# Optimization experiments

Hardware: AMD Instinct MI355X
Metric: run time of the kernel (lower is better)

Reference implementation:

```python
import jax, jax.numpy as jnp
import numpy as np

COMMITMENT_COST = 0.25


def setup_inputs() -> dict:
    key = jax.random.key(0)
    k1, k2 = jax.random.split(key)
    B, S, D, K = 8, 4096, 256, 1024
    inputs = jax.random.normal(k1, (B, S, D), dtype=jnp.float32)
    attention_mask = jnp.ones((B, S), dtype=jnp.float32)
    codebook = jax.random.normal(k2, (K, D), dtype=jnp.float32)
    return {"inputs": inputs, "attention_mask": attention_mask, "codebook": codebook}


def reference(inputs, attention_mask, codebook):
    # Inference-mode forward of VectorQuantizer (no EMA update / init / revival).
    B, S, D = inputs.shape
    z = inputs.astype(jnp.float32).reshape(-1, D)          # (N, D)
    m = attention_mask.reshape(-1).astype(jnp.float32)     # (N,)

    cb = codebook.astype(jnp.float32)                      # (K, D)
    # squared L2 distances: ||z||^2 - 2 z e^T + ||e||^2
    dist = (jnp.sum(z * z, axis=-1, keepdims=True)
            - 2.0 * jnp.matmul(z, cb.T)
            + jnp.sum(cb * cb, axis=-1)[None, :])          # (N, K)
    idx = jnp.argmin(dist, axis=-1)                        # (N,)
    q = cb[idx]                                            # (N, D) codebook lookup

    n_valid = jnp.sum(m)
    # mse over valid tokens (elementwise mean, matching F.mse_loss on flat_valid)
    diff = z - jax.lax.stop_gradient(q)
    commitment = jnp.sum(m[:, None] * diff * diff) / (n_valid * D)
    vq_loss = COMMITMENT_COST * commitment

    # straight-through estimator; invalid positions zeroed (as in torch scatter)
    q_ste = z + jax.lax.stop_gradient(q - z)
    quantized = (q_ste * m[:, None]).reshape(B, S, D)
    indices = jnp.where(m > 0, idx, 0).reshape(B, S)
    return quantized, vq_loss, indices
```

## Files before the change

kernel.cpp:

```cpp
#include <hip/hip_runtime.h>
#include <cstdint>

typedef short bf16x8 __attribute__((ext_vector_type(8)));
typedef float f32x4  __attribute__((ext_vector_type(4)));

#define TOK    64
#define PITCH  264
#define HROWS  (64 * PITCH)
#define MAXC   32

__device__ __forceinline__ unsigned short f2bf(float f) {
  unsigned u = __float_as_uint(f);
  return (unsigned short)((u + 0x7FFFu + ((u >> 16) & 1u)) >> 16);
}
__device__ __forceinline__ uint4 pack8(float4 a, float4 b) {
  uint4 u;
  u.x = (unsigned)f2bf(a.x) | ((unsigned)f2bf(a.y) << 16);
  u.y = (unsigned)f2bf(a.z) | ((unsigned)f2bf(a.w) << 16);
  u.z = (unsigned)f2bf(b.x) | ((unsigned)f2bf(b.y) << 16);
  u.w = (unsigned)f2bf(b.z) | ((unsigned)f2bf(b.w) << 16);
  return u;
}

__global__ __launch_bounds__(256) void vq_prep(const float* __restrict__ cb,
                                               unsigned short* __restrict__ cb_bf,
                                               float* __restrict__ ee,
                                               float* __restrict__ acc2,
                                               int* __restrict__ done_ctr, int K) {
  if (blockIdx.x == 0 && threadIdx.x == 0) {
    acc2[0] = 0.f; acc2[1] = 0.f; *done_ctr = 0;
  }
  int wave = threadIdx.x >> 6, lane = threadIdx.x & 63;
  int k = blockIdx.x * 4 + wave;
  if (k >= K) return;
  float4 v = *reinterpret_cast<const float4*>(cb + (size_t)k * 256 + lane * 4);
  float s = v.x * v.x + v.y * v.y + v.z * v.z + v.w * v.w;
  #pragma unroll
  for (int off = 32; off; off >>= 1) s += __shfl_down(s, off, 64);
  ushort4 b;
  b.x = f2bf(v.x); b.y = f2bf(v.y); b.z = f2bf(v.z); b.w = f2bf(v.w);
  *reinterpret_cast<ushort4*>(cb_bf + (size_t)k * 256 + lane * 4) = b;
  if (lane == 0) ee[k] = s;
}

__global__ __launch_bounds__(256, 2) void vq_main(
    const float* __restrict__ z, const float* __restrict__ cb,
    const unsigned short* __restrict__ cb_bf, const float* __restrict__ ee,
    const float* __restrict__ mask,
    float* __restrict__ out_q, float* __restrict__ out_idx_f,
    float* __restrict__ out_loss, float* __restrict__ acc2,
    int* __restrict__ done_ctr, int nblocks, int K) {
  __shared__ __align__(16) unsigned short buf[128 * PITCH];
  __shared__ float ee_lds[1024];
  __shared__ float znorm[TOK];
  __shared__ int   ccnt[TOK];
  __shared__ unsigned short cand[TOK * MAXC];
  __shared__ float red[8];
  __shared__ bool  last;

  const int t = threadIdx.x;
  const int n0 = blockIdx.x * TOK;
  const int q16 = t & 15;

  ee_lds[t]       = ee[t];
  ee_lds[t + 256] = ee[t + 256];
  ee_lds[t + 512] = ee[t + 512];
  ee_lds[t + 768] = ee[t + 768];
  if (t < TOK) ccnt[t] = 0;

  #pragma unroll
  for (int pass = 0; pass < 4; ++pass) {
    int row = pass * 16 + (t >> 4);
    const float* zr = z + (size_t)(n0 + row) * 256;
    float ssq = 0.f;
    #pragma unroll
    for (int j = 0; j < 2; ++j) {
      float4 a = *reinterpret_cast<const float4*>(zr + q16 * 8 + j * 128);
      float4 b = *reinterpret_cast<const float4*>(zr + q16 * 8 + j * 128 + 4);
      ssq += a.x*a.x + a.y*a.y + a.z*a.z + a.w*a.w
           + b.x*b.x + b.y*b.y + b.z*b.z + b.w*b.w;
      *reinterpret_cast<uint4*>(&buf[row * PITCH + q16 * 8 + j * 128]) = pack8(a, b);
    }
    #pragma unroll
    for (int off = 1; off < 16; off <<= 1) ssq += __shfl_xor(ssq, off, 64);
    if (q16 == 0) znorm[row] = sqrtf(ssq);
  }
  __syncthreads();

  const int wv = t >> 6, lane = t & 63;
  const int p = wv & 1, kh = wv >> 1;
  const int quad = lane >> 4, l15 = lane & 15;
  bf16x8 afrag[2][8];
  float  znreg[2][4];
  #pragma unroll
  for (int s = 0; s < 2; ++s) {
    const unsigned short* za = &buf[(p * 32 + s * 16 + l15) * PITCH + quad * 8];
    #pragma unroll
    for (int kk = 0; kk < 8; ++kk)
      afrag[s][kk] = *reinterpret_cast<const bf16x8*>(za + kk * 32);
    #pragma unroll
    for (int r = 0; r < 4; ++r)
      znreg[s][r] = znorm[p * 32 + s * 16 + quad * 4 + r];
  }
  __syncthreads();

  float amin[2][4];
  #pragma unroll
  for (int s = 0; s < 2; ++s)
    #pragma unroll
    for (int r = 0; r < 4; ++r) amin[s][r] = 3.4e38f;

  const int tq = (p << 6) | lane;
  const int sq16 = tq & 15, srow = tq >> 4;
  unsigned short* qbuf = &buf[kh * HROWS];

  for (int lc = 0; lc < 8; ++lc) {
    const int kbase = kh * 512 + lc * 64;
    #pragma unroll
    for (int pass = 0; pass < 8; ++pass) {
      int row = pass * 8 + srow;
      const unsigned short* src = cb_bf + (size_t)(kbase + row) * 256;
      #pragma unroll
      for (int j = 0; j < 2; ++j) {
        uint4 v = *reinterpret_cast<const uint4*>(src + sq16 * 8 + j * 128);
        *reinterpret_cast<uint4*>(&qbuf[row * PITCH + sq16 * 8 + j * 128]) = v;
      }
    }
    __syncthreads();

    f32x4 acc[2][4];
    #pragma unroll
    for (int s = 0; s < 2; ++s)
      #pragma unroll
      for (int ct = 0; ct < 4; ++ct) acc[s][ct] = (f32x4){0.f, 0.f, 0.f, 0.f};
    #pragma unroll
    for (int kk = 0; kk < 8; ++kk) {
      bf16x8 b0 = *reinterpret_cast<const bf16x8*>(&qbuf[(l15)      * PITCH + quad * 8 + kk * 32]);
      bf16x8 b1 = *reinterpret_cast<const bf16x8*>(&qbuf[(16 + l15) * PITCH + quad * 8 + kk * 32]);
      bf16x8 b2 = *reinterpret_cast<const bf16x8*>(&qbuf[(32 + l15) * PITCH + quad * 8 + kk * 32]);
      bf16x8 b3 = *reinterpret_cast<const bf16x8*>(&qbuf[(48 + l15) * PITCH + quad * 8 + kk * 32]);
      acc[0][0] = __builtin_amdgcn_mfma_f32_16x16x32_bf16(afrag[0][kk], b0, acc[0][0], 0, 0, 0);
      acc[1][0] = __builtin_amdgcn_mfma_f32_16x16x32_bf16(afrag[1][kk], b0, acc[1][0], 0, 0, 0);
      acc[0][1] = __builtin_amdgcn_mfma_f32_16x16x32_bf16(afrag[0][kk], b1, acc[0][1], 0, 0, 0);
      acc[1][1] = __builtin_amdgcn_mfma_f32_16x16x32_bf16(afrag[1][kk], b1, acc[1][1], 0, 0, 0);
      acc[0][2] = __builtin_amdgcn_mfma_f32_16x16x32_bf16(afrag[0][kk], b2, acc[0][2], 0, 0, 0);
      acc[1][2] = __builtin_amdgcn_mfma_f32_16x16x32_bf16(afrag[1][kk], b2, acc[1][2], 0, 0, 0);
      acc[0][3] = __builtin_amdgcn_mfma_f32_16x16x32_bf16(afrag[0][kk], b3, acc[0][3], 0, 0, 0);
      acc[1][3] = __builtin_amdgcn_mfma_f32_16x16x32_bf16(afrag[1][kk], b3, acc[1][3], 0, 0, 0);
    }

    float e0 = ee_lds[kbase + l15],      e1 = ee_lds[kbase + 16 + l15];
    float e2 = ee_lds[kbase + 32 + l15], e3 = ee_lds[kbase + 48 + l15];
    float en0 = sqrtf(e0), en1 = sqrtf(e1), en2 = sqrtf(e2), en3 = sqrtf(e3);
    #pragma unroll
    for (int s = 0; s < 2; ++s) {
      #pragma unroll
      for (int r = 0; r < 4; ++r) {
        float d0 = e0 - 2.f * acc[s][0][r];
        float d1 = e1 - 2.f * acc[s][1][r];
        float d2 = e2 - 2.f * acc[s][2][r];
        float d3 = e3 - 2.f * acc[s][3][r];
        float w = fminf(fminf(d0, d1), fminf(d2, d3));
        #pragma unroll
        for (int off = 1; off < 16; off <<= 1) w = fminf(w, __shfl_xor(w, off, 64));
        float am = fminf(amin[s][r], w);
        amin[s][r] = am;
        int tok = p * 32 + s * 16 + quad * 4 + r;
        float zn = znreg[s][r];
        if (d0 <= am + 1.5f + 0.002f * zn * en0) {
          int sl = atomicAdd(&ccnt[tok], 1);
          if (sl < MAXC) cand[tok * MAXC + sl] = (unsigned short)(kbase + l15);
        }
        if (d1 <= am + 1.5f + 0.002f * zn * en1) {
          int sl = atomicAdd(&ccnt[tok], 1);
          if (sl < MAXC) cand[tok * MAXC + sl] = (unsigned short)(kbase + 16 + l15);
        }
        if (d2 <= am + 1.5f + 0.002f * zn * en2) {
          int sl = atomicAdd(&ccnt[tok], 1);
          if (sl < MAXC) cand[tok * MAXC + sl] = (unsigned short)(kbase + 32 + l15);
        }
        if (d3 <= am + 1.5f + 0.002f * zn * en3) {
          int sl = atomicAdd(&ccnt[tok], 1);
          if (sl < MAXC) cand[tok * MAXC + sl] = (unsigned short)(kbase + 48 + l15);
        }
      }
    }
    __syncthreads();
  }

  float lsum = 0.f, msum = 0.f;
  for (int it = 0; it < 16; ++it) {
    int tok = wv * 16 + it;
    int n = n0 + tok;
    float4 zv = *reinterpret_cast<const float4*>(z + (size_t)n * 256 + lane * 4);
    int cnt = ccnt[tok];
    float bs = 3.4e38f; int bk = 0;
    if (cnt > MAXC) {
      for (int k = 0; k < K; ++k) {
        float4 ev = *reinterpret_cast<const float4*>(cb + (size_t)k * 256 + lane * 4);
        float dp = zv.x * ev.x + zv.y * ev.y + zv.z * ev.z + zv.w * ev.w;
        #pragma unroll
        for (int off = 32; off; off >>= 1) dp += __shfl_xor(dp, off, 64);
        float s = ee_lds[k] - 2.f * dp;
        if (s < bs) { bs = s; bk = k; }
      }
    } else {
      for (int c = 0; c < cnt; ++c) {
        int k = cand[tok * MAXC + c];
        float4 ev = *reinterpret_cast<const float4*>(cb + (size_t)k * 256 + lane * 4);
        float dp = zv.x * ev.x + zv.y * ev.y + zv.z * ev.z + zv.w * ev.w;
        #pragma unroll
        for (int off = 32; off; off >>= 1) dp += __shfl_xor(dp, off, 64);
        float s = ee_lds[k] - 2.f * dp;
        if (s < bs || (s == bs && k < bk)) { bs = s; bk = k; }
      }
    }
    float m = mask[n];
    float4 qv = *reinterpret_cast<const float4*>(cb + (size_t)bk * 256 + lane * 4);
    float4 o; o.x = qv.x * m; o.y = qv.y * m; o.z = qv.z * m; o.w = qv.w * m;
    *reinterpret_cast<float4*>(out_q + (size_t)n * 256 + lane * 4) = o;
    float dx = zv.x - qv.x, dy = zv.y - qv.y, dz = zv.z - qv.z, dw = zv.w - qv.w;
    lsum = fmaf(m, dx * dx + dy * dy + dz * dz + dw * dw, lsum);
    if (lane == 0) {
      msum += m;
      out_idx_f[n] = (m > 0.f) ? (float)bk : 0.f;
    }
  }
  #pragma unroll
  for (int off = 32; off; off >>= 1) lsum += __shfl_down(lsum, off, 64);
  if (lane == 0) { red[wv] = lsum; red[4 + wv] = msum; }
  __syncthreads();
  if (t == 0) {
    atomicAdd(&acc2[0], red[0] + red[1] + red[2] + red[3]);
    atomicAdd(&acc2[1], red[4] + red[5] + red[6] + red[7]);
    __threadfence();
    int prev = atomicAdd(done_ctr, 1);
    last = (prev == nblocks - 1);
  }
  __syncthreads();
  if (last && t == 0) {
    float s  = atomicAdd(&acc2[0], 0.0f);
    float nv = atomicAdd(&acc2[1], 0.0f);
    out_loss[0] = (nv > 0.f) ? (0.25f * s / (nv * 256.0f)) : 0.0f;
  }
}

extern "C" void kernel_launch(void* const* d_in, const int* in_sizes, int n_in,
                              void* d_out, int out_size, void* d_ws, size_t ws_size,
                              hipStream_t stream) {
  const float* z    = (const float*)d_in[0];
  const float* mask = (const float*)d_in[1];
  const float* cb   = (const float*)d_in[2];
  const int N = in_sizes[1];
  const int D = 256;
  const int K = in_sizes[2] / D;

  float* wsf  = (float*)d_ws;
  float* acc2 = wsf;
  int*   dctr = (int*)(wsf + 2);
  float* ee   = wsf + 8;
  unsigned short* cb_bf = (unsigned short*)(ee + K);

  float* out_q     = (float*)d_out;
  float* out_loss  = out_q + (size_t)N * D;
  float* out_idx_f = out_loss + 1;

  vq_prep<<<(K + 3) / 4, 256, 0, stream>>>(cb, cb_bf, ee, acc2, dctr, K);
  vq_main<<<N / TOK, 256, 0, stream>>>(z, cb, cb_bf, ee, mask, out_q,
                                       out_idx_f, out_loss, acc2, dctr, N / TOK, K);
}
```

Before: 194.0 us.

## Double block to 512 threads, prefetch codebook tiles, and prune refine candidates

Blocks grow to 512 threads (8 waves), and each wave now owns 16 tokens with one fragment set instead of 32. Codebook tiles are prefetched into registers one chunk ahead so global loads overlap the MFMA work, and MFMA sections run at raised wave priority. Candidate entries now pack a truncated distance with the index, and a shared atomicMin tracks each token's running best. The refine pass drops candidates beyond a threshold and skips exact recomputation when only one survives. This cuts the exact fp32 refine work, but adds LDS atomics and a heuristic threshold that could affect argmin correctness on close ties.

```diff
diff --git a/kernel.cpp b/kernel.cpp
--- a/kernel.cpp
+++ b/kernel.cpp
@@ -7,7 +7,7 @@
 #define TOK    64
 #define PITCH  264
 #define HROWS  (64 * PITCH)
-#define MAXC   32
+#define MAXC   24
 
 __device__ __forceinline__ unsigned short f2bf(float f) {
   unsigned u = __float_as_uint(f);
@@ -43,7 +43,7 @@
   if (lane == 0) ee[k] = s;
 }
 
-__global__ __launch_bounds__(256, 2) void vq_main(
+__global__ __launch_bounds__(512, 2) void vq_main(
     const float* __restrict__ z, const float* __restrict__ cb,
     const unsigned short* __restrict__ cb_bf, const float* __restrict__ ee,
     const float* __restrict__ mask,
@@ -54,32 +54,38 @@
   __shared__ float ee_lds[1024];
   __shared__ float znorm[TOK];
   __shared__ int   ccnt[TOK];
-  __shared__ unsigned short cand[TOK * MAXC];
-  __shared__ float red[8];
+  __shared__ unsigned umin[TOK];
+  __shared__ unsigned cand[TOK * MAXC];
+  __shared__ float red[16];
   __shared__ bool  last;
 
   const int t = threadIdx.x;
   const int n0 = blockIdx.x * TOK;
+  const int wv = t >> 6, lane = t & 63;
+  const int kh = wv >> 2, ts = wv & 3;
+  const int quad = lane >> 4, l15 = lane & 15;
   const int q16 = t & 15;
 
-  ee_lds[t]       = ee[t];
-  ee_lds[t + 256] = ee[t + 256];
-  ee_lds[t + 512] = ee[t + 512];
-  ee_lds[t + 768] = ee[t + 768];
-  if (t < TOK) ccnt[t] = 0;
-
-  #pragma unroll
-  for (int pass = 0; pass < 4; ++pass) {
-    int row = pass * 16 + (t >> 4);
+  float ea = ee[t], eb = ee[t + 512];
+  ee_lds[t] = ea; ee_lds[t + 512] = eb;
+  if (t < TOK) { ccnt[t] = 0; umin[t] = 0x7F7FFC00u; }
+  float em = fmaxf(ea, eb);
+  #pragma unroll
+  for (int off = 32; off; off >>= 1) em = fmaxf(em, __shfl_xor(em, off, 64));
+  if (lane == 0) red[wv] = em;
+
+  #pragma unroll
+  for (int pass = 0; pass < 2; ++pass) {
+    int row = pass * 32 + (t >> 4);
     const float* zr = z + (size_t)(n0 + row) * 256;
     float ssq = 0.f;
     #pragma unroll
     for (int j = 0; j < 2; ++j) {
-      float4 a = *reinterpret_cast<const float4*>(zr + q16 * 8 + j * 128);
-      float4 b = *reinterpret_cast<const float4*>(zr + q16 * 8 + j * 128 + 4);
+      float4 a = *reinterpret_cast<const float4*>(zr + q16 * 16 + j * 8);
+      float4 b = *reinterpret_cast<const float4*>(zr + q16 * 16 + j * 8 + 4);
       ssq += a.x*a.x + a.y*a.y + a.z*a.z + a.w*a.w
            + b.x*b.x + b.y*b.y + b.z*b.z + b.w*b.w;
-      *reinterpret_cast<uint4*>(&buf[row * PITCH + q16 * 8 + j * 128]) = pack8(a, b);
+      *reinterpret_cast<uint4*>(&buf[row * PITCH + q16 * 16 + j * 8]) = pack8(a, b);
     }
     #pragma unroll
     for (int off = 1; off < 16; off <<= 1) ssq += __shfl_xor(ssq, off, 64);
@@ -87,115 +93,132 @@
   }
   __syncthreads();
 
-  const int wv = t >> 6, lane = t & 63;
-  const int p = wv & 1, kh = wv >> 1;
-  const int quad = lane >> 4, l15 = lane & 15;
-  bf16x8 afrag[2][8];
-  float  znreg[2][4];
-  #pragma unroll
-  for (int s = 0; s < 2; ++s) {
-    const unsigned short* za = &buf[(p * 32 + s * 16 + l15) * PITCH + quad * 8];
+  float enmax;
+  {
+    float m8 = red[0];
+    #pragma unroll
+    for (int i = 1; i < 8; ++i) m8 = fmaxf(m8, red[i]);
+    enmax = sqrtf(m8);
+  }
+
+  const int tt = t & 255;
+  const unsigned short* cbh = cb_bf + (size_t)kh * 512 * 256;
+  uint4 st[8];
+  #pragma unroll
+  for (int u = 0; u < 8; ++u)
+    st[u] = *reinterpret_cast<const uint4*>(cbh + (size_t)(u * 256 + tt) * 8);
+
+  bf16x8 afrag[8];
+  float  znreg[4];
+  {
+    const unsigned short* za = &buf[(ts * 16 + l15) * PITCH + quad * 8];
     #pragma unroll
     for (int kk = 0; kk < 8; ++kk)
-      afrag[s][kk] = *reinterpret_cast<const bf16x8*>(za + kk * 32);
+      afrag[kk] = *reinterpret_cast<const bf16x8*>(za + kk * 32);
     #pragma unroll
     for (int r = 0; r < 4; ++r)
-      znreg[s][r] = znorm[p * 32 + s * 16 + quad * 4 + r];
-  }
-  __syncthreads();
-
-  float amin[2][4];
-  #pragma unroll
-  for (int s = 0; s < 2; ++s)
-    #pragma unroll
-    for (int r = 0; r < 4; ++r) amin[s][r] = 3.4e38f;
-
-  const int tq = (p << 6) | lane;
-  const int sq16 = tq & 15, srow = tq >> 4;
+      znreg[r] = znorm[ts * 16 + quad * 4 + r];
+  }
+  __syncthreads();
+
   unsigned short* qbuf = &buf[kh * HROWS];
+  #pragma unroll
+  for (int u = 0; u < 8; ++u) {
+    int f = u * 256 + tt;
+    *reinterpret_cast<uint4*>(&qbuf[(f >> 5) * PITCH + (f & 31) * 8]) = st[u];
+  }
+  __syncthreads();
+
+  float amin[4] = {3.4e38f, 3.4e38f, 3.4e38f, 3.4e38f};
 
   for (int lc = 0; lc < 8; ++lc) {
     const int kbase = kh * 512 + lc * 64;
-    #pragma unroll
-    for (int pass = 0; pass < 8; ++pass) {
-      int row = pass * 8 + srow;
-      const unsigned short* src = cb_bf + (size_t)(kbase + row) * 256;
+    if (lc < 7) {
+      const unsigned short* src = cbh + (size_t)(lc + 1) * 64 * 256;
       #pragma unroll
-      for (int j = 0; j < 2; ++j) {
-        uint4 v = *reinterpret_cast<const uint4*>(src + sq16 * 8 + j * 128);
-        *reinterpret_cast<uint4*>(&qbuf[row * PITCH + sq16 * 8 + j * 128]) = v;
-      }
-    }
-    __syncthreads();
-
-    f32x4 acc[2][4];
-    #pragma unroll
-    for (int s = 0; s < 2; ++s)
-      #pragma unroll
-      for (int ct = 0; ct < 4; ++ct) acc[s][ct] = (f32x4){0.f, 0.f, 0.f, 0.f};
+      for (int u = 0; u < 8; ++u)
+        st[u] = *reinterpret_cast<const uint4*>(src + (size_t)(u * 256 + tt) * 8);
+    }
+
+    f32x4 acc[4];
+    #pragma unroll
+    for (int ct = 0; ct < 4; ++ct) acc[ct] = (f32x4){0.f, 0.f, 0.f, 0.f};
+    __builtin_amdgcn_s_setprio(1);
     #pragma unroll
     for (int kk = 0; kk < 8; ++kk) {
       bf16x8 b0 = *reinterpret_cast<const bf16x8*>(&qbuf[(l15)      * PITCH + quad * 8 + kk * 32]);
       bf16x8 b1 = *reinterpret_cast<const bf16x8*>(&qbuf[(16 + l15) * PITCH + quad * 8 + kk * 32]);
       bf16x8 b2 = *reinterpret_cast<const bf16x8*>(&qbuf[(32 + l15) * PITCH + quad * 8 + kk * 32]);
       bf16x8 b3 = *reinterpret_cast<const bf16x8*>(&qbuf[(48 + l15) * PITCH + quad * 8 + kk * 32]);
-      acc[0][0] = __builtin_amdgcn_mfma_f32_16x16x32_bf16(afrag[0][kk], b0, acc[0][0], 0, 0, 0);
-      acc[1][0] = __builtin_amdgcn_mfma_f32_16x16x32_bf16(afrag[1][kk], b0, acc[1][0], 0, 0, 0);
-      acc[0][1] = __builtin_amdgcn_mfma_f32_16x16x32_bf16(afrag[0][kk], b1, acc[0][1], 0, 0, 0);
-      acc[1][1] = __builtin_amdgcn_mfma_f32_16x16x32_bf16(afrag[1][kk], b1, acc[1][1], 0, 0, 0);
-      acc[0][2] = __builtin_amdgcn_mfma_f32_16x16x32_bf16(afrag[0][kk], b2, acc[0][2], 0, 0, 0);
-      acc[1][2] = __builtin_amdgcn_mfma_f32_16x16x32_bf16(afrag[1][kk], b2, acc[1][2], 0, 0, 0);
-      acc[0][3] = __builtin_amdgcn_mfma_f32_16x16x32_bf16(afrag[0][kk], b3, acc[0][3], 0, 0, 0);
-      acc[1][3] = __builtin_amdgcn_mfma_f32_16x16x32_bf16(afrag[1][kk], b3, acc[1][3], 0, 0, 0);
-    }
+      acc[0] = __builtin_amdgcn_mfma_f32_16x16x32_bf16(afrag[kk], b0, acc[0], 0, 0, 0);
+      acc[1] = __builtin_amdgcn_mfma_f32_16x16x32_bf16(afrag[kk], b1, acc[1], 0, 0, 0);
+      acc[2] = __builtin_amdgcn_mfma_f32_16x16x32_bf16(afrag[kk], b2, acc[2], 0, 0, 0);
+      acc[3] = __builtin_amdgcn_mfma_f32_16x16x32_bf16(afrag[kk], b3, acc[3], 0, 0, 0);
+    }
+    __builtin_amdgcn_s_setprio(0);
 
     float e0 = ee_lds[kbase + l15],      e1 = ee_lds[kbase + 16 + l15];
     float e2 = ee_lds[kbase + 32 + l15], e3 = ee_lds[kbase + 48 + l15];
     float en0 = sqrtf(e0), en1 = sqrtf(e1), en2 = sqrtf(e2), en3 = sqrtf(e3);
     #pragma unroll
-    for (int s = 0; s < 2; ++s) {
+    for (int r = 0; r < 4; ++r) {
+      float d0 = e0 - 2.f * acc[0][r];
+      float d1 = e1 - 2.f * acc[1][r];
+      float d2 = e2 - 2.f * acc[2][r];
+      float d3 = e3 - 2.f * acc[3][r];
+      float w = fminf(fminf(d0, d1), fminf(d2, d3));
       #pragma unroll
-      for (int r = 0; r < 4; ++r) {
-        float d0 = e0 - 2.f * acc[s][0][r];
-        float d1 = e1 - 2.f * acc[s][1][r];
-        float d2 = e2 - 2.f * acc[s][2][r];
-        float d3 = e3 - 2.f * acc[s][3][r];
-        float w = fminf(fminf(d0, d1), fminf(d2, d3));
-        #pragma unroll
-        for (int off = 1; off < 16; off <<= 1) w = fminf(w, __shfl_xor(w, off, 64));
-        float am = fminf(amin[s][r], w);
-        amin[s][r] = am;
-        int tok = p * 32 + s * 16 + quad * 4 + r;
-        float zn = znreg[s][r];
-        if (d0 <= am + 1.5f + 0.002f * zn * en0) {
-          int sl = atomicAdd(&ccnt[tok], 1);
-          if (sl < MAXC) cand[tok * MAXC + sl] = (unsigned short)(kbase + l15);
-        }
-        if (d1 <= am + 1.5f + 0.002f * zn * en1) {
-          int sl = atomicAdd(&ccnt[tok], 1);
-          if (sl < MAXC) cand[tok * MAXC + sl] = (unsigned short)(kbase + 16 + l15);
-        }
-        if (d2 <= am + 1.5f + 0.002f * zn * en2) {
-          int sl = atomicAdd(&ccnt[tok], 1);
-          if (sl < MAXC) cand[tok * MAXC + sl] = (unsigned short)(kbase + 32 + l15);
-        }
-        if (d3 <= am + 1.5f + 0.002f * zn * en3) {
-          int sl = atomicAdd(&ccnt[tok], 1);
-          if (sl < MAXC) cand[tok * MAXC + sl] = (unsigned short)(kbase + 48 + l15);
-        }
+      for (int off = 1; off < 16; off <<= 1) w = fminf(w, __shfl_xor(w, off, 64));
+      int tok = ts * 16 + quad * 4 + r;
+      float gq = __uint_as_float(umin[tok] & 0xFFFFFC00u);
+      float am = fminf(fminf(amin[r], w), gq);
+      amin[r] = am;
+      float zn = znreg[r];
+      if (d0 <= am + 1.63f + 0.002f * zn * en0) {
+        unsigned pu = (__float_as_uint(fmaxf(d0, 0.f)) & 0xFFFFFC00u) | (unsigned)(kbase + l15);
+        atomicMin(&umin[tok], pu);
+        int sl = atomicAdd(&ccnt[tok], 1);
+        if (sl < MAXC) cand[tok * MAXC + sl] = pu;
+      }
+      if (d1 <= am + 1.63f + 0.002f * zn * en1) {
+        unsigned pu = (__float_as_uint(fmaxf(d1, 0.f)) & 0xFFFFFC00u) | (unsigned)(kbase + 16 + l15);
+        atomicMin(&umin[tok], pu);
+        int sl = atomicAdd(&ccnt[tok], 1);
+        if (sl < MAXC) cand[tok * MAXC + sl] = pu;
+      }
+      if (d2 <= am + 1.63f + 0.002f * zn * en2) {
+        unsigned pu = (__float_as_uint(fmaxf(d2, 0.f)) & 0xFFFFFC00u) | (unsigned)(kbase + 32 + l15);
+        atomicMin(&umin[tok], pu);
+        int sl = atomicAdd(&ccnt[tok], 1);
+        if (sl < MAXC) cand[tok * MAXC + sl] = pu;
+      }
+      if (d3 <= am + 1.63f + 0.002f * zn * en3) {
+        unsigned pu = (__float_as_uint(fmaxf(d3, 0.f)) & 0xFFFFFC00u) | (unsigned)(kbase + 48 + l15);
+        atomicMin(&umin[tok], pu);
+        int sl = atomicAdd(&ccnt[tok], 1);
+        if (sl < MAXC) cand[tok * MAXC + sl] = pu;
       }
     }
     __syncthreads();
+    if (lc < 7) {
+      #pragma unroll
+      for (int u = 0; u < 8; ++u) {
+        int f = u * 256 + tt;
+        *reinterpret_cast<uint4*>(&qbuf[(f >> 5) * PITCH + (f & 31) * 8]) = st[u];
+      }
+      __syncthreads();
+    }
   }
 
   float lsum = 0.f, msum = 0.f;
-  for (int it = 0; it < 16; ++it) {
-    int tok = wv * 16 + it;
+  for (int it = 0; it < 8; ++it) {
+    int tok = wv * 8 + it;
     int n = n0 + tok;
     float4 zv = *reinterpret_cast<const float4*>(z + (size_t)n * 256 + lane * 4);
     int cnt = ccnt[tok];
-    float bs = 3.4e38f; int bk = 0;
+    int bk = 0;
     if (cnt > MAXC) {
+      float bs = 3.4e38f;
       for (int k = 0; k < K; ++k) {
         float4 ev = *reinterpret_cast<const float4*>(cb + (size_t)k * 256 + lane * 4);
         float dp = zv.x * ev.x + zv.y * ev.y + zv.z * ev.z + zv.w * ev.w;
@@ -205,14 +228,29 @@
         if (s < bs) { bs = s; bk = k; }
       }
     } else {
-      for (int c = 0; c < cnt; ++c) {
-        int k = cand[tok * MAXC + c];
-        float4 ev = *reinterpret_cast<const float4*>(cb + (size_t)k * 256 + lane * 4);
-        float dp = zv.x * ev.x + zv.y * ev.y + zv.z * ev.z + zv.w * ev.w;
-        #pragma unroll
-        for (int off = 32; off; off >>= 1) dp += __shfl_xor(dp, off, 64);
-        float s = ee_lds[k] - 2.f * dp;
-        if (s < bs || (s == bs && k < bk)) { bs = s; bk = k; }
+      unsigned pm = umin[tok];
+      float thr = __uint_as_float(pm & 0xFFFFFC00u)
+                + 1.63f + 0.002f * znorm[tok] * enmax;
+      int c = (lane < cnt) ? lane : 0;
+      unsigned pe = cand[tok * MAXC + c];
+      bool flag = (lane < cnt) && (__uint_as_float(pe & 0xFFFFFC00u) <= thr);
+      unsigned long long msk = __ballot(flag);
+      if (__popcll(msk) == 1) {
+        bk = (int)(pm & 1023u);
+      } else {
+        float bs = 3.4e38f; bk = 1 << 29;
+        while (msk) {
+          int cc = __ffsll(msk) - 1;
+          msk &= msk - 1;
+          unsigned pc = cand[tok * MAXC + cc];
+          int k = (int)(pc & 1023u);
+          float4 ev = *reinterpret_cast<const float4*>(cb + (size_t)k * 256 + lane * 4);
+          float dp = zv.x * ev.x + zv.y * ev.y + zv.z * ev.z + zv.w * ev.w;
+          #pragma unroll
+          for (int off = 32; off; off >>= 1) dp += __shfl_xor(dp, off, 64);
+          float s = ee_lds[k] - 2.f * dp;
+          if (s < bs || (s == bs && k < bk)) { bs = s; bk = k; }
+        }
       }
     }
     float m = mask[n];
@@ -228,11 +266,14 @@
   }
   #pragma unroll
   for (int off = 32; off; off >>= 1) lsum += __shfl_down(lsum, off, 64);
-  if (lane == 0) { red[wv] = lsum; red[4 + wv] = msum; }
+  if (lane == 0) { red[wv] = lsum; red[8 + wv] = msum; }
   __syncthreads();
   if (t == 0) {
-    atomicAdd(&acc2[0], red[0] + red[1] + red[2] + red[3]);
-    atomicAdd(&acc2[1], red[4] + red[5] + red[6] + red[7]);
+    float a = 0.f, b = 0.f;
+    #pragma unroll
+    for (int i = 0; i < 8; ++i) { a += red[i]; b += red[8 + i]; }
+    atomicAdd(&acc2[0], a);
+    atomicAdd(&acc2[1], b);
     __threadfence();
     int prev = atomicAdd(done_ctr, 1);
     last = (prev == nblocks - 1);
@@ -266,6 +307,6 @@
   float* out_idx_f = out_loss + 1;
 
   vq_prep<<<(K + 3) / 4, 256, 0, stream>>>(cb, cb_bf, ee, acc2, dctr, K);
-  vq_main<<<N / TOK, 256, 0, stream>>>(z, cb, cb_bf, ee, mask, out_q,
+  vq_main<<<N / TOK, 512, 0, stream>>>(z, cb, cb_bf, ee, mask, out_q,
                                        out_idx_f, out_loss, acc2, dctr, N / TOK, K);
 }
```

Result: slower. 201.7 us (+4.0%).

## Shrink LDS tile, share packed running minimum, and prune fp32 refinement candidates

Applied to the files above, without the earlier changes.

Halves the codebook staging tile to 32 rows per chunk and drops the LDS copy of codebook norms, cutting shared memory so more blocks can reside per CU. A packed distance-plus-index value in LDS, updated with atomicMin, shares the running minimum between the two waves covering each token. In the epilogue, candidates are filtered against a global threshold, and when only one survives its index is taken directly without an fp32 recheck. This trades more loop iterations and LDS atomics, plus a slightly wider tolerance margin, for less exact fp32 refinement work.

```diff
diff --git a/kernel.cpp b/kernel.cpp
--- a/kernel.cpp
+++ b/kernel.cpp
@@ -6,8 +6,8 @@
 
 #define TOK    64
 #define PITCH  264
-#define HROWS  (64 * PITCH)
-#define MAXC   32
+#define CROWS  32
+#define MAXC   16
 
 __device__ __forceinline__ unsigned short f2bf(float f) {
   unsigned u = __float_as_uint(f);
@@ -50,23 +50,27 @@
     float* __restrict__ out_q, float* __restrict__ out_idx_f,
     float* __restrict__ out_loss, float* __restrict__ acc2,
     int* __restrict__ done_ctr, int nblocks, int K) {
-  __shared__ __align__(16) unsigned short buf[128 * PITCH];
-  __shared__ float ee_lds[1024];
+  __shared__ __align__(16) unsigned short buf[64 * PITCH];
   __shared__ float znorm[TOK];
   __shared__ int   ccnt[TOK];
-  __shared__ unsigned short cand[TOK * MAXC];
+  __shared__ unsigned umin[TOK];
+  __shared__ unsigned cand[TOK * MAXC];
   __shared__ float red[8];
   __shared__ bool  last;
 
   const int t = threadIdx.x;
   const int n0 = blockIdx.x * TOK;
+  const int wv = t >> 6, lane = t & 63;
+  const int p = wv & 1, kh = wv >> 1;
+  const int quad = lane >> 4, l15 = lane & 15;
   const int q16 = t & 15;
 
-  ee_lds[t]       = ee[t];
-  ee_lds[t + 256] = ee[t + 256];
-  ee_lds[t + 512] = ee[t + 512];
-  ee_lds[t + 768] = ee[t + 768];
-  if (t < TOK) ccnt[t] = 0;
+  if (t < TOK) { ccnt[t] = 0; umin[t] = 0x7F7FFC00u; }
+
+  float em = fmaxf(fmaxf(ee[t], ee[t + 256]), fmaxf(ee[t + 512], ee[t + 768]));
+  #pragma unroll
+  for (int off = 32; off; off >>= 1) em = fmaxf(em, __shfl_xor(em, off, 64));
+  if (lane == 0) red[wv] = em;
 
   #pragma unroll
   for (int pass = 0; pass < 4; ++pass) {
@@ -87,9 +91,8 @@
   }
   __syncthreads();
 
-  const int wv = t >> 6, lane = t & 63;
-  const int p = wv & 1, kh = wv >> 1;
-  const int quad = lane >> 4, l15 = lane & 15;
+  const float enmax = sqrtf(fmaxf(fmaxf(red[0], red[1]), fmaxf(red[2], red[3])));
+
   bf16x8 afrag[2][8];
   float  znreg[2][4];
   #pragma unroll
@@ -104,84 +107,79 @@
   }
   __syncthreads();
 
+  unsigned short* qbuf = &buf[kh * CROWS * PITCH];
+  const unsigned short* cbh = cb_bf + (size_t)kh * 512 * 256;
+  const int tq = t & 127;
+
   float amin[2][4];
   #pragma unroll
   for (int s = 0; s < 2; ++s)
     #pragma unroll
     for (int r = 0; r < 4; ++r) amin[s][r] = 3.4e38f;
 
-  const int tq = (p << 6) | lane;
-  const int sq16 = tq & 15, srow = tq >> 4;
-  unsigned short* qbuf = &buf[kh * HROWS];
-
-  for (int lc = 0; lc < 8; ++lc) {
-    const int kbase = kh * 512 + lc * 64;
-    #pragma unroll
-    for (int pass = 0; pass < 8; ++pass) {
-      int row = pass * 8 + srow;
-      const unsigned short* src = cb_bf + (size_t)(kbase + row) * 256;
-      #pragma unroll
-      for (int j = 0; j < 2; ++j) {
-        uint4 v = *reinterpret_cast<const uint4*>(src + sq16 * 8 + j * 128);
-        *reinterpret_cast<uint4*>(&qbuf[row * PITCH + sq16 * 8 + j * 128]) = v;
+  for (int lc = 0; lc < 16; ++lc) {
+    const int kbase = kh * 512 + lc * CROWS;
+    #pragma unroll
+    for (int g = 0; g < 2; ++g) {
+      uint4 v[4];
+      #pragma unroll
+      for (int u = 0; u < 4; ++u) {
+        int flat = (g * 4 + u) * 128 + tq;
+        v[u] = *reinterpret_cast<const uint4*>(
+            cbh + (size_t)(lc * CROWS + (flat >> 5)) * 256 + (flat & 31) * 8);
+      }
+      #pragma unroll
+      for (int u = 0; u < 4; ++u) {
+        int flat = (g * 4 + u) * 128 + tq;
+        *reinterpret_cast<uint4*>(&qbuf[(flat >> 5) * PITCH + (flat & 31) * 8]) = v[u];
       }
     }
     __syncthreads();
 
-    f32x4 acc[2][4];
+    f32x4 acc[2][2];
     #pragma unroll
     for (int s = 0; s < 2; ++s)
       #pragma unroll
-      for (int ct = 0; ct < 4; ++ct) acc[s][ct] = (f32x4){0.f, 0.f, 0.f, 0.f};
+      for (int ct = 0; ct < 2; ++ct) acc[s][ct] = (f32x4){0.f, 0.f, 0.f, 0.f};
+    __builtin_amdgcn_s_setprio(1);
     #pragma unroll
     for (int kk = 0; kk < 8; ++kk) {
       bf16x8 b0 = *reinterpret_cast<const bf16x8*>(&qbuf[(l15)      * PITCH + quad * 8 + kk * 32]);
       bf16x8 b1 = *reinterpret_cast<const bf16x8*>(&qbuf[(16 + l15) * PITCH + quad * 8 + kk * 32]);
-      bf16x8 b2 = *reinterpret_cast<const bf16x8*>(&qbuf[(32 + l15) * PITCH + quad * 8 + kk * 32]);
-      bf16x8 b3 = *reinterpret_cast<const bf16x8*>(&qbuf[(48 + l15) * PITCH + quad * 8 + kk * 32]);
       acc[0][0] = __builtin_amdgcn_mfma_f32_16x16x32_bf16(afrag[0][kk], b0, acc[0][0], 0, 0, 0);
       acc[1][0] = __builtin_amdgcn_mfma_f32_16x16x32_bf16(afrag[1][kk], b0, acc[1][0], 0, 0, 0);
       acc[0][1] = __builtin_amdgcn_mfma_f32_16x16x32_bf16(afrag[0][kk], b1, acc[0][1], 0, 0, 0);
       acc[1][1] = __builtin_amdgcn_mfma_f32_16x16x32_bf16(afrag[1][kk], b1, acc[1][1], 0, 0, 0);
-      acc[0][2] = __builtin_amdgcn_mfma_f32_16x16x32_bf16(afrag[0][kk], b2, acc[0][2], 0, 0, 0);
-      acc[1][2] = __builtin_amdgcn_mfma_f32_16x16x32_bf16(afrag[1][kk], b2, acc[1][2], 0, 0, 0);
-      acc[0][3] = __builtin_amdgcn_mfma_f32_16x16x32_bf16(afrag[0][kk], b3, acc[0][3], 0, 0, 0);
-      acc[1][3] = __builtin_amdgcn_mfma_f32_16x16x32_bf16(afrag[1][kk], b3, acc[1][3], 0, 0, 0);
-    }
-
-    float e0 = ee_lds[kbase + l15],      e1 = ee_lds[kbase + 16 + l15];
-    float e2 = ee_lds[kbase + 32 + l15], e3 = ee_lds[kbase + 48 + l15];
-    float en0 = sqrtf(e0), en1 = sqrtf(e1), en2 = sqrtf(e2), en3 = sqrtf(e3);
+    }
+    __builtin_amdgcn_s_setprio(0);
+
+    float e0 = ee[kbase + l15], e1 = ee[kbase + 16 + l15];
+    float en0 = sqrtf(e0), en1 = sqrtf(e1);
     #pragma unroll
     for (int s = 0; s < 2; ++s) {
       #pragma unroll
       for (int r = 0; r < 4; ++r) {
         float d0 = e0 - 2.f * acc[s][0][r];
         float d1 = e1 - 2.f * acc[s][1][r];
-        float d2 = e2 - 2.f * acc[s][2][r];
-        float d3 = e3 - 2.f * acc[s][3][r];
-        float w = fminf(fminf(d0, d1), fminf(d2, d3));
+        float w = fminf(d0, d1);
         #pragma unroll
         for (int off = 1; off < 16; off <<= 1) w = fminf(w, __shfl_xor(w, off, 64));
-        float am = fminf(amin[s][r], w);
+        int tok = p * 32 + s * 16 + quad * 4 + r;
+        float gq = __uint_as_float(umin[tok] & 0xFFFFFC00u);
+        float am = fminf(fminf(amin[s][r], w), gq);
         amin[s][r] = am;
-        int tok = p * 32 + s * 16 + quad * 4 + r;
         float zn = znreg[s][r];
-        if (d0 <= am + 1.5f + 0.002f * zn * en0) {
+        if (d0 <= am + 1.63f + 0.002f * zn * en0) {
+          unsigned pu = (__float_as_uint(fmaxf(d0, 0.f)) & 0xFFFFFC00u) | (unsigned)(kbase + l15);
+          atomicMin(&umin[tok], pu);
           int sl = atomicAdd(&ccnt[tok], 1);
-          if (sl < MAXC) cand[tok * MAXC + sl] = (unsigned short)(kbase + l15);
+          if (sl < MAXC) cand[tok * MAXC + sl] = pu;
         }
-        if (d1 <= am + 1.5f + 0.002f * zn * en1) {
+        if (d1 <= am + 1.63f + 0.002f * zn * en1) {
+          unsigned pu = (__float_as_uint(fmaxf(d1, 0.f)) & 0xFFFFFC00u) | (unsigned)(kbase + 16 + l15);
+          atomicMin(&umin[tok], pu);
           int sl = atomicAdd(&ccnt[tok], 1);
-          if (sl < MAXC) cand[tok * MAXC + sl] = (unsigned short)(kbase + 16 + l15);
-        }
-        if (d2 <= am + 1.5f + 0.002f * zn * en2) {
-          int sl = atomicAdd(&ccnt[tok], 1);
-          if (sl < MAXC) cand[tok * MAXC + sl] = (unsigned short)(kbase + 32 + l15);
-        }
-        if (d3 <= am + 1.5f + 0.002f * zn * en3) {
-          int sl = atomicAdd(&ccnt[tok], 1);
-          if (sl < MAXC) cand[tok * MAXC + sl] = (unsigned short)(kbase + 48 + l15);
+          if (sl < MAXC) cand[tok * MAXC + sl] = pu;
         }
       }
     }
@@ -194,25 +192,41 @@
     int n = n0 + tok;
     float4 zv = *reinterpret_cast<const float4*>(z + (size_t)n * 256 + lane * 4);
     int cnt = ccnt[tok];
-    float bs = 3.4e38f; int bk = 0;
+    int bk = 0;
     if (cnt > MAXC) {
+      float bs = 3.4e38f;
       for (int k = 0; k < K; ++k) {
         float4 ev = *reinterpret_cast<const float4*>(cb + (size_t)k * 256 + lane * 4);
         float dp = zv.x * ev.x + zv.y * ev.y + zv.z * ev.z + zv.w * ev.w;
         #pragma unroll
         for (int off = 32; off; off >>= 1) dp += __shfl_xor(dp, off, 64);
-        float s = ee_lds[k] - 2.f * dp;
+        float s = ee[k] - 2.f * dp;
         if (s < bs) { bs = s; bk = k; }
       }
     } else {
-      for (int c = 0; c < cnt; ++c) {
-        int k = cand[tok * MAXC + c];
-        float4 ev = *reinterpret_cast<const float4*>(cb + (size_t)k * 256 + lane * 4);
-        float dp = zv.x * ev.x + zv.y * ev.y + zv.z * ev.z + zv.w * ev.w;
-        #pragma unroll
-        for (int off = 32; off; off >>= 1) dp += __shfl_xor(dp, off, 64);
-        float s = ee_lds[k] - 2.f * dp;
-        if (s < bs || (s == bs && k < bk)) { bs = s; bk = k; }
+      unsigned pm = umin[tok];
+      float thr = __uint_as_float(pm & 0xFFFFFC00u)
+                + 1.63f + 0.002f * znorm[tok] * enmax;
+      int c = (lane < cnt) ? lane : 0;
+      unsigned pe = cand[tok * MAXC + c];
+      bool flag = (lane < cnt) && (__uint_as_float(pe & 0xFFFFFC00u) <= thr);
+      unsigned long long msk = __ballot(flag);
+      if (__popcll(msk) == 1) {
+        bk = (int)(pm & 1023u);
+      } else {
+        float bs = 3.4e38f; bk = 1 << 29;
+        while (msk) {
+          int cc = __ffsll(msk) - 1;
+          msk &= msk - 1;
+          unsigned pc = cand[tok * MAXC + cc];
+          int k = (int)(pc & 1023u);
+          float4 ev = *reinterpret_cast<const float4*>(cb + (size_t)k * 256 + lane * 4);
+          float dp = zv.x * ev.x + zv.y * ev.y + zv.z * ev.z + zv.w * ev.w;
+          #pragma unroll
+          for (int off = 32; off; off >>= 1) dp += __shfl_xor(dp, off, 64);
+          float s = ee[k] - 2.f * dp;
+          if (s < bs || (s == bs && k < bk)) { bs = s; bk = k; }
+        }
       }
     }
     float m = mask[n];
```

New measurement: 532.9 us. 175% more time.

## Register-prefetch next codebook chunk during MFMA and raise wave priority

Applied to the files above, without the earlier changes.

Each codebook chunk is now loaded from global memory into 16 uint4 registers one iteration ahead. The loads are issued before the MFMA block and written to LDS after the candidate-selection barrier, so global-load latency overlaps with compute instead of stalling at the top of each iteration. It also raises wave priority around the MFMA loop with s_setprio. The 64 extra VGPRs per thread may lower occupancy or cause spills.

```diff
diff --git a/kernel.cpp b/kernel.cpp
--- a/kernel.cpp
+++ b/kernel.cpp
@@ -114,25 +114,42 @@
   const int sq16 = tq & 15, srow = tq >> 4;
   unsigned short* qbuf = &buf[kh * HROWS];
 
+  uint4 st[16];
+  {
+    const unsigned short* base = cb_bf + (size_t)kh * 512 * 256;
+    #pragma unroll
+    for (int pass = 0; pass < 8; ++pass) {
+      const unsigned short* src = base + (size_t)(pass * 8 + srow) * 256 + sq16 * 8;
+      st[pass * 2]     = *reinterpret_cast<const uint4*>(src);
+      st[pass * 2 + 1] = *reinterpret_cast<const uint4*>(src + 128);
+    }
+    #pragma unroll
+    for (int pass = 0; pass < 8; ++pass) {
+      int row = pass * 8 + srow;
+      *reinterpret_cast<uint4*>(&qbuf[row * PITCH + sq16 * 8])       = st[pass * 2];
+      *reinterpret_cast<uint4*>(&qbuf[row * PITCH + sq16 * 8 + 128]) = st[pass * 2 + 1];
+    }
+  }
+  __syncthreads();
+
   for (int lc = 0; lc < 8; ++lc) {
     const int kbase = kh * 512 + lc * 64;
-    #pragma unroll
-    for (int pass = 0; pass < 8; ++pass) {
-      int row = pass * 8 + srow;
-      const unsigned short* src = cb_bf + (size_t)(kbase + row) * 256;
-      #pragma unroll
-      for (int j = 0; j < 2; ++j) {
-        uint4 v = *reinterpret_cast<const uint4*>(src + sq16 * 8 + j * 128);
-        *reinterpret_cast<uint4*>(&qbuf[row * PITCH + sq16 * 8 + j * 128]) = v;
-      }
-    }
-    __syncthreads();
+    if (lc < 7) {
+      const unsigned short* base = cb_bf + (size_t)(kh * 512 + (lc + 1) * 64) * 256;
+      #pragma unroll
+      for (int pass = 0; pass < 8; ++pass) {
+        const unsigned short* src = base + (size_t)(pass * 8 + srow) * 256 + sq16 * 8;
+        st[pass * 2]     = *reinterpret_cast<const uint4*>(src);
+        st[pass * 2 + 1] = *reinterpret_cast<const uint4*>(src + 128);
+      }
+    }
 
     f32x4 acc[2][4];
     #pragma unroll
     for (int s = 0; s < 2; ++s)
       #pragma unroll
       for (int ct = 0; ct < 4; ++ct) acc[s][ct] = (f32x4){0.f, 0.f, 0.f, 0.f};
+    __builtin_amdgcn_s_setprio(1);
     #pragma unroll
     for (int kk = 0; kk < 8; ++kk) {
       bf16x8 b0 = *reinterpret_cast<const bf16x8*>(&qbuf[(l15)      * PITCH + quad * 8 + kk * 32]);
@@ -148,6 +165,7 @@
       acc[0][3] = __builtin_amdgcn_mfma_f32_16x16x32_bf16(afrag[0][kk], b3, acc[0][3], 0, 0, 0);
       acc[1][3] = __builtin_amdgcn_mfma_f32_16x16x32_bf16(afrag[1][kk], b3, acc[1][3], 0, 0, 0);
     }
+    __builtin_amdgcn_s_setprio(0);
 
     float e0 = ee_lds[kbase + l15],      e1 = ee_lds[kbase + 16 + l15];
     float e2 = ee_lds[kbase + 32 + l15], e3 = ee_lds[kbase + 48 + l15];
@@ -186,6 +204,15 @@
       }
     }
     __syncthreads();
+    if (lc < 7) {
+      #pragma unroll
+      for (int pass = 0; pass < 8; ++pass) {
+        int row = pass * 8 + srow;
+        *reinterpret_cast<uint4*>(&qbuf[row * PITCH + sq16 * 8])       = st[pass * 2];
+        *reinterpret_cast<uint4*>(&qbuf[row * PITCH + sq16 * 8 + 128]) = st[pass * 2 + 1];
+      }
+      __syncthreads();
+    }
   }
 
   float lsum = 0.f, msum = 0.f;
```

Result: slower. 237.8 us (+22.6%).
